# Kernel tuning notes

Hardware: AMD Instinct MI355X
Metric: run time of the kernel (lower is better)

The kernel has to match this reference:

```python
import jax, jax.numpy as jnp
import numpy as np

N_NODES = 100000
N_EDGES = 3200000
IN_DIM = 512
HID_DIM = 16


def spmm(edge_src, edge_dst, edge_weight, feats):
    # out[i] = sum_{(j->i) in E} w_e * feats[j]  (sparse adj @ feats)
    gathered = feats[edge_src] * edge_weight[:, None]  # [E, D]
    return jax.ops.segment_sum(gathered, edge_dst, num_segments=N_NODES)


def setup_inputs() -> dict:
    key = jax.random.key(0)
    ks = jax.random.split(key, 8)
    x = jax.random.normal(ks[0], (N_NODES, IN_DIM), dtype=jnp.float32)
    edge_src = jax.random.randint(ks[1], (N_EDGES,), 0, N_NODES, dtype=jnp.int32)
    edge_dst = jax.random.randint(ks[2], (N_EDGES,), 0, N_NODES, dtype=jnp.int32)
    # normalized adjacency weights (positive, small, like D^-1/2 A D^-1/2 entries)
    edge_weight = jax.random.uniform(ks[3], (N_EDGES,), dtype=jnp.float32) * 0.1
    # Glorot-style init for GraphConvolution weights
    W1 = jax.random.normal(ks[4], (IN_DIM, HID_DIM), dtype=jnp.float32) * (1.0 / np.sqrt(IN_DIM))
    b1 = jnp.zeros((HID_DIM,), dtype=jnp.float32)
    W2 = jax.random.normal(ks[5], (HID_DIM, 1), dtype=jnp.float32) * (1.0 / np.sqrt(HID_DIM))
    b2 = jnp.zeros((1,), dtype=jnp.float32)
    return {"x": x, "edge_src": edge_src, "edge_dst": edge_dst,
            "edge_weight": edge_weight, "W1": W1, "b1": b1, "W2": W2, "b2": b2}


def reference(x, edge_src, edge_dst, edge_weight, W1, b1, W2, b2):
    # Layer 1: GraphConvolution(input_dim -> hidden_dim) + ReLU
    h = spmm(edge_src, edge_dst, edge_weight, x @ W1) + b1  # [N, 16]
    h = jax.nn.relu(h)
    # dropout is identity in eval mode (training=False)
    # Layer 2: GraphConvolution(hidden_dim -> 1)
    out = spmm(edge_src, edge_dst, edge_weight, h @ W2) + b2  # [N, 1]
    return out
```

## Files before the change

### kernel.cpp

```cpp
#include <hip/hip_runtime.h>
#include <hip/hip_fp16.h>

#define N_NODES 100000
#define N_EDGES 3200000
#define IN_DIM  512
#define HID_DIM 16

#define B_BKT   782
#define BKT_SH  7
#define EPB2    5000
#define NBLK2   640
#define CAP_MAX 4608
#define RSTG    9

#define G1_TILES 6250
#define G1_BLK   782
#define MERGED_SMEM 61440

typedef __attribute__((ext_vector_type(8))) short bf16x8;
typedef __attribute__((ext_vector_type(4))) float f32x4;

__device__ __forceinline__ void atomic_add_f32(float* p, float v) {
    __hip_atomic_fetch_add(p, v, __ATOMIC_RELAXED, __HIP_MEMORY_SCOPE_AGENT);
}
__device__ __forceinline__ int atomic_add_i32(int* p, int v) {
    return __hip_atomic_fetch_add(p, v, __ATOMIC_RELAXED, __HIP_MEMORY_SCOPE_AGENT);
}

__device__ __forceinline__ unsigned short bf16_rne(float f) {
    unsigned u = __float_as_uint(f);
    return (unsigned short)((u + 0x7fffu + ((u >> 16) & 1u)) >> 16);
}

__device__ __forceinline__ short bhi(float f) {
    return (short)(__float_as_uint(f) >> 16);
}
__device__ __forceinline__ short blo(float f) {
    float hif = __uint_as_float(__float_as_uint(f) & 0xffff0000u);
    return (short)bf16_rne(f - hif);
}

__device__ __forceinline__ void cvt_hilo(float4 u, float4 v,
                                         bf16x8* __restrict__ hi,
                                         bf16x8* __restrict__ lo) {
    bf16x8 h, l;
    h[0] = bhi(u.x); h[1] = bhi(u.y); h[2] = bhi(u.z); h[3] = bhi(u.w);
    h[4] = bhi(v.x); h[5] = bhi(v.y); h[6] = bhi(v.z); h[7] = bhi(v.w);
    l[0] = blo(u.x); l[1] = blo(u.y); l[2] = blo(u.z); l[3] = blo(u.w);
    l[4] = blo(v.x); l[5] = blo(v.y); l[6] = blo(v.z); l[7] = blo(v.w);
    *hi = h; *lo = l;
}

__device__ __forceinline__ void g1_tile_body(const float* __restrict__ xrow,
                                             const unsigned short* __restrict__ whp,
                                             const unsigned short* __restrict__ wlp,
                                             __half* __restrict__ xwh,
                                             int row0, int lane) {
    f32x4 acc = {0.f, 0.f, 0.f, 0.f};
    float4 a0 = *(const float4*)(xrow);
    float4 a1 = *(const float4*)(xrow + 4);
    float4 b0 = *(const float4*)(xrow + 32);
    float4 b1 = *(const float4*)(xrow + 36);
#pragma unroll
    for (int i = 0; i < 8; ++i) {
        float4 n0, n1, m0, m1;
        if (i < 7) {
            n0 = *(const float4*)(xrow + (2 * i + 2) * 32);
            n1 = *(const float4*)(xrow + (2 * i + 2) * 32 + 4);
            m0 = *(const float4*)(xrow + (2 * i + 3) * 32);
            m1 = *(const float4*)(xrow + (2 * i + 3) * 32 + 4);
        }
        bf16x8 ah, al;
        cvt_hilo(a0, a1, &ah, &al);
        bf16x8 bh = *(const bf16x8*)(whp + (size_t)(2 * i) * 512);
        bf16x8 bl = *(const bf16x8*)(wlp + (size_t)(2 * i) * 512);
        acc = __builtin_amdgcn_mfma_f32_16x16x32_bf16(ah, bh, acc, 0, 0, 0);
        acc = __builtin_amdgcn_mfma_f32_16x16x32_bf16(al, bh, acc, 0, 0, 0);
        acc = __builtin_amdgcn_mfma_f32_16x16x32_bf16(ah, bl, acc, 0, 0, 0);
        cvt_hilo(b0, b1, &ah, &al);
        bh = *(const bf16x8*)(whp + (size_t)(2 * i + 1) * 512);
        bl = *(const bf16x8*)(wlp + (size_t)(2 * i + 1) * 512);
        acc = __builtin_amdgcn_mfma_f32_16x16x32_bf16(ah, bh, acc, 0, 0, 0);
        acc = __builtin_amdgcn_mfma_f32_16x16x32_bf16(al, bh, acc, 0, 0, 0);
        acc = __builtin_amdgcn_mfma_f32_16x16x32_bf16(ah, bl, acc, 0, 0, 0);
        a0 = n0; a1 = n1; b0 = m0; b1 = m1;
    }
    const int n     = lane & 15;
    const int rbase = row0 + ((lane >> 4) << 2);
    xwh[(size_t)(rbase + 0) * HID_DIM + n] = __float2half_rn(acc[0]);
    xwh[(size_t)(rbase + 1) * HID_DIM + n] = __float2half_rn(acc[1]);
    xwh[(size_t)(rbase + 2) * HID_DIM + n] = __float2half_rn(acc[2]);
    xwh[(size_t)(rbase + 3) * HID_DIM + n] = __float2half_rn(acc[3]);
}

__global__ void z0_init(int* __restrict__ cursor, int cap) {
    int b = blockIdx.x * blockDim.x + threadIdx.x;
    if (b < B_BKT) cursor[b] = b * cap;
}

__global__ __launch_bounds__(512) void m1_gs(const float* __restrict__ x,
                                             const float* __restrict__ W1,
                                             __half* __restrict__ xwh,
                                             const int* __restrict__ src,
                                             const int* __restrict__ dst,
                                             const float* __restrict__ wgt,
                                             int* __restrict__ cursor,
                                             uint2* __restrict__ rec, int cap) {
    extern __shared__ __align__(16) char smem[];
    const int t = threadIdx.x;

    if (blockIdx.x < NBLK2) {
        uint2*          srt   = (uint2*)smem;
        unsigned short* bkt   = (unsigned short*)(smem + 40000);
        int*            hist  = (int*)(smem + 50000);
        int*            lbase = (int*)(smem + 53128);
        int*            gbase = (int*)(smem + 56256);
        int*            scn   = (int*)(smem + 59384);

        for (int b = t; b < B_BKT; b += 512) hist[b] = 0;
        __syncthreads();

        const int e0 = blockIdx.x * EPB2;
        const int4*   d4 = (const int4*)(dst + e0);
        const int4*   s4 = (const int4*)(src + e0);
        const float4* w4 = (const float4*)(wgt + e0);
        const int NG = EPB2 / 4;

        for (int g = t; g < NG; g += 512) {
            int4 d = d4[g];
            atomicAdd(&hist[d.x >> BKT_SH], 1);
            atomicAdd(&hist[d.y >> BKT_SH], 1);
            atomicAdd(&hist[d.z >> BKT_SH], 1);
            atomicAdd(&hist[d.w >> BKT_SH], 1);
        }
        __syncthreads();

        int c0 = 0, c1 = 0;
        if (t < 391) { c0 = hist[2 * t]; c1 = hist[2 * t + 1]; }
        int s = c0 + c1;
        scn[t] = s;
        __syncthreads();
        for (int off = 1; off < 512; off <<= 1) {
            int v = (t >= off) ? scn[t - off] : 0;
            __syncthreads();
            scn[t] += v;
            __syncthreads();
        }
        int excl = scn[t] - s;
        if (t < 391) {
            lbase[2 * t]     = excl;
            lbase[2 * t + 1] = excl + c0;
        }
        __syncthreads();

        for (int b = t; b < B_BKT; b += 512) {
            int c = hist[b];
            gbase[b] = c > 0 ? atomic_add_i32(&cursor[b], c) : 0;
        }
        __syncthreads();
        for (int b = t; b < B_BKT; b += 512) hist[b] = lbase[b];
        __syncthreads();

        for (int g = t; g < NG; g += 512) {
            int4 d = d4[g];
            int4 sv = s4[g];
            float4 w = w4[g];
            {
                int b = d.x >> BKT_SH;
                int pos = atomicAdd(&hist[b], 1);
                srt[pos] = make_uint2(((unsigned)sv.x << BKT_SH) | (unsigned)(d.x & 127),
                                      __float_as_uint(w.x));
                bkt[pos] = (unsigned short)b;
            }
            {
                int b = d.y >> BKT_SH;
                int pos = atomicAdd(&hist[b], 1);
                srt[pos] = make_uint2(((unsigned)sv.y << BKT_SH) | (unsigned)(d.y & 127),
                                      __float_as_uint(w.y));
                bkt[pos] = (unsigned short)b;
            }
            {
                int b = d.z >> BKT_SH;
                int pos = atomicAdd(&hist[b], 1);
                srt[pos] = make_uint2(((unsigned)sv.z << BKT_SH) | (unsigned)(d.z & 127),
                                      __float_as_uint(w.z));
                bkt[pos] = (unsigned short)b;
            }
            {
                int b = d.w >> BKT_SH;
                int pos = atomicAdd(&hist[b], 1);
                srt[pos] = make_uint2(((unsigned)sv.w << BKT_SH) | (unsigned)(d.w & 127),
                                      __float_as_uint(w.w));
                bkt[pos] = (unsigned short)b;
            }
        }
        __syncthreads();

        for (int i = t; i < EPB2; i += 512) {
            int b = bkt[i];
            rec[gbase[b] + (i - lbase[b])] = srt[i];
        }
    } else {
        unsigned short* whi = (unsigned short*)smem;
        unsigned short* wlo = (unsigned short*)(smem + 16384);

        for (int idx = t; idx < 16 * 64 * 8; idx += 512) {
            int c  = idx >> 9;
            int l  = (idx >> 3) & 63;
            int tt = idx & 7;
            int k  = c * 32 + ((l >> 4) << 3) + tt;
            int j  = l & 15;
            float w = W1[k * HID_DIM + j];
            unsigned u = __float_as_uint(w);
            float hif = __uint_as_float(u & 0xffff0000u);
            whi[idx] = (unsigned short)(u >> 16);
            wlo[idx] = bf16_rne(w - hif);
        }
        __syncthreads();

        const int lane = t & 63;
        const int wid  = (blockIdx.x - NBLK2) * 8 + (t >> 6);
        if (wid >= G1_TILES) return;
        const int row0 = wid * 16;

        const float* xrow = x + (size_t)(row0 + (lane & 15)) * IN_DIM + ((lane >> 4) << 3);
        g1_tile_body(xrow, &whi[lane * 8], &wlo[lane * 8], xwh, row0, lane);
    }
}

__global__ __launch_bounds__(256) void g1_xw_mfma(const float* __restrict__ x,
                                                  const float* __restrict__ W1,
                                                  __half* __restrict__ xwh) {
    __shared__ alignas(16) unsigned short whi[16 * 64 * 8];
    __shared__ alignas(16) unsigned short wlo[16 * 64 * 8];
    const int t = threadIdx.x;

    for (int idx = t; idx < 16 * 64 * 8; idx += 256) {
        int c  = idx >> 9;
        int l  = (idx >> 3) & 63;
        int tt = idx & 7;
        int k  = c * 32 + ((l >> 4) << 3) + tt;
        int j  = l & 15;
        float w = W1[k * HID_DIM + j];
        unsigned u = __float_as_uint(w);
        float hif = __uint_as_float(u & 0xffff0000u);
        whi[idx] = (unsigned short)(u >> 16);
        wlo[idx] = bf16_rne(w - hif);
    }
    __syncthreads();

    const int lane = t & 63;
    const int wid  = blockIdx.x * 4 + (t >> 6);
    if (wid >= G1_TILES) return;
    const int row0 = wid * 16;

    const float* xrow = x + (size_t)(row0 + (lane & 15)) * IN_DIM + ((lane >> 4) << 3);
    g1_tile_body(xrow, &whi[lane * 8], &wlo[lane * 8], xwh, row0, lane);
}

__global__ __launch_bounds__(512) void s2p4b(const int* __restrict__ cursor,
                                             const uint2* __restrict__ rec,
                                             const __half* __restrict__ xwh,
                                             const float* __restrict__ b1,
                                             const float* __restrict__ W2,
                                             float* __restrict__ hw, int cap) {
    __shared__ uint2 srt[CAP_MAX];
    __shared__ int ocnt[128], scn[128], cur[128];
    const int t = threadIdx.x;
    const int bkt = blockIdx.x;
    const int e0 = bkt * cap;
    int n = cursor[bkt] - e0;
    n = max(0, min(n, cap));
    if (t < 128) ocnt[t] = 0;
    __syncthreads();

    uint2 rg[RSTG];
#pragma unroll
    for (int q = 0; q < RSTG; ++q) {
        int i = t + q * 512;
        if (i < n) {
            rg[q] = rec[e0 + i];
            atomicAdd(&ocnt[rg[q].x & 127u], 1);
        }
    }
    __syncthreads();

    if (t < 128) scn[t] = ocnt[t];
    __syncthreads();
    for (int off = 1; off < 128; off <<= 1) {
        int v = 0;
        if (t < 128 && t >= off) v = scn[t - off];
        __syncthreads();
        if (t < 128 && t >= off) scn[t] += v;
        __syncthreads();
    }
    if (t < 128) cur[t] = scn[t] - ocnt[t];
    __syncthreads();

#pragma unroll
    for (int q = 0; q < RSTG; ++q) {
        int i = t + q * 512;
        if (i < n) {
            uint2 r = rg[q];
            int d = (int)(r.x & 127u);
            int pos = atomicAdd(&cur[d], 1);
            srt[pos] = make_uint2(r.x >> BKT_SH, r.y);
        }
    }
    __syncthreads();

    const int j = t & 15;
    for (int g = (t >> 4); g < 128; g += 32) {
        const int node = (bkt << BKT_SH) + g;
        if (node >= N_NODES) continue;
        int e = scn[g] - ocnt[g];
        const int end = scn[g];
        float acc = 0.0f;
        for (; e + 8 <= end; e += 8) {
            uint2 q0 = srt[e],     q1 = srt[e + 1], q2 = srt[e + 2], q3 = srt[e + 3];
            uint2 q4 = srt[e + 4], q5 = srt[e + 5], q6 = srt[e + 6], q7 = srt[e + 7];
            float f0 = __half2float(xwh[(size_t)q0.x * HID_DIM + j]);
            float f1 = __half2float(xwh[(size_t)q1.x * HID_DIM + j]);
            float f2 = __half2float(xwh[(size_t)q2.x * HID_DIM + j]);
            float f3 = __half2float(xwh[(size_t)q3.x * HID_DIM + j]);
            float f4 = __half2float(xwh[(size_t)q4.x * HID_DIM + j]);
            float f5 = __half2float(xwh[(size_t)q5.x * HID_DIM + j]);
            float f6 = __half2float(xwh[(size_t)q6.x * HID_DIM + j]);
            float f7 = __half2float(xwh[(size_t)q7.x * HID_DIM + j]);
            acc += __uint_as_float(q0.y) * f0;
            acc += __uint_as_float(q1.y) * f1;
            acc += __uint_as_float(q2.y) * f2;
            acc += __uint_as_float(q3.y) * f3;
            acc += __uint_as_float(q4.y) * f4;
            acc += __uint_as_float(q5.y) * f5;
            acc += __uint_as_float(q6.y) * f6;
            acc += __uint_as_float(q7.y) * f7;
        }
        for (; e + 4 <= end; e += 4) {
            uint2 q0 = srt[e], q1 = srt[e + 1], q2 = srt[e + 2], q3 = srt[e + 3];
            float f0 = __half2float(xwh[(size_t)q0.x * HID_DIM + j]);
            float f1 = __half2float(xwh[(size_t)q1.x * HID_DIM + j]);
            float f2 = __half2float(xwh[(size_t)q2.x * HID_DIM + j]);
            float f3 = __half2float(xwh[(size_t)q3.x * HID_DIM + j]);
            acc += __uint_as_float(q0.y) * f0;
            acc += __uint_as_float(q1.y) * f1;
            acc += __uint_as_float(q2.y) * f2;
            acc += __uint_as_float(q3.y) * f3;
        }
        for (; e < end; ++e) {
            uint2 q = srt[e];
            acc += __uint_as_float(q.y) * __half2float(xwh[(size_t)q.x * HID_DIM + j]);
        }
        float v = fmaxf(acc + b1[j], 0.0f) * W2[j];
        v += __shfl_xor(v, 1);
        v += __shfl_xor(v, 2);
        v += __shfl_xor(v, 4);
        v += __shfl_xor(v, 8);
        if (j == 0) hw[node] = v;
    }
}

__global__ __launch_bounds__(512) void p5c(const int* __restrict__ cursor,
                                           const uint2* __restrict__ rec,
                                           const float* __restrict__ hwv,
                                           const float* __restrict__ b2,
                                           float* __restrict__ out, int cap) {
    __shared__ float o[128];
    const int t = threadIdx.x;
    const int bkt = blockIdx.x;
    const int e0 = bkt * cap;
    int n = cursor[bkt] - e0;
    n = max(0, min(n, cap));
    if (t < 128) o[t] = 0.0f;
    __syncthreads();
    const uint4* r4 = (const uint4*)(rec + e0);
    const int m = n >> 1;
    for (int i = t; i < m; i += 512) {
        uint4 q = r4[i];
        float v0 = __uint_as_float(q.y) * hwv[q.x >> BKT_SH];
        float v1 = __uint_as_float(q.w) * hwv[q.z >> BKT_SH];
        atomicAdd(&o[q.x & 127u], v0);
        atomicAdd(&o[q.z & 127u], v1);
    }
    if ((n & 1) && t == 0) {
        uint2 q = rec[e0 + n - 1];
        atomicAdd(&o[q.x & 127u], __uint_as_float(q.y) * hwv[q.x >> BKT_SH]);
    }
    __syncthreads();
    if (t < 128) {
        int node = (bkt << BKT_SH) + t;
        if (node < N_NODES) out[node] = b2[0] + o[t];
    }
}

__global__ void f0_zero(float* __restrict__ h, const float* __restrict__ b2,
                        float* __restrict__ out) {
    int i = blockIdx.x * blockDim.x + threadIdx.x;
    if (i < N_NODES * HID_DIM) h[i] = 0.0f;
    if (i < N_NODES) out[i] = b2[0];
}
__global__ void k2_spmm1(const int* __restrict__ src, const int* __restrict__ dst,
                         const float* __restrict__ wgt, const __half* __restrict__ xwh,
                         float* __restrict__ h) {
    int t = blockIdx.x * blockDim.x + threadIdx.x;
    int e = t >> 4;
    int j = t & (HID_DIM - 1);
    if (e < N_EDGES) {
        float v = wgt[e] * __half2float(xwh[(size_t)src[e] * HID_DIM + j]);
        atomic_add_f32(&h[(size_t)dst[e] * HID_DIM + j], v);
    }
}
__global__ void k3_act(const float* __restrict__ h, const float* __restrict__ b1,
                       const float* __restrict__ W2, float* __restrict__ hw) {
    int i = blockIdx.x * blockDim.x + threadIdx.x;
    if (i >= N_NODES) return;
    const float4* h4 = (const float4*)(h + (size_t)i * HID_DIM);
    const float4* b4 = (const float4*)b1;
    const float4* w4 = (const float4*)W2;
    float acc = 0.0f;
#pragma unroll
    for (int q = 0; q < HID_DIM / 4; ++q) {
        float4 hv = h4[q]; float4 bv = b4[q]; float4 wv = w4[q];
        acc += fmaxf(hv.x + bv.x, 0.0f) * wv.x;
        acc += fmaxf(hv.y + bv.y, 0.0f) * wv.y;
        acc += fmaxf(hv.z + bv.z, 0.0f) * wv.z;
        acc += fmaxf(hv.w + bv.w, 0.0f) * wv.w;
    }
    hw[i] = acc;
}
__global__ void k4_spmm2(const int* __restrict__ src, const int* __restrict__ dst,
                         const float* __restrict__ wgt, const float* __restrict__ hw,
                         float* __restrict__ out) {
    int e = blockIdx.x * blockDim.x + threadIdx.x;
    if (e < N_EDGES) atomic_add_f32(&out[dst[e]], wgt[e] * hw[src[e]]);
}


extern "C" void kernel_launch(void* const* d_in, const int* in_sizes, int n_in,
                              void* d_out, int out_size, void* d_ws, size_t ws_size,
                              hipStream_t stream) {
    const float* x    = (const float*)d_in[0];
    const int*   esrc = (const int*)  d_in[1];
    const int*   edst = (const int*)  d_in[2];
    const float* ew   = (const float*)d_in[3];
    const float* W1   = (const float*)d_in[4];
    const float* b1   = (const float*)d_in[5];
    const float* W2   = (const float*)d_in[6];
    const float* b2   = (const float*)d_in[7];
    float* out = (float*)d_out;
    char* ws = (char*)d_ws;

    __half* xwh    = (__half*)ws;
    float*  hw     = (float*)(ws + (size_t)N_NODES * HID_DIM * 2);
    int*    cursor = (int*)(hw + N_NODES);
    int2*   row    = (int2*)(((size_t)(cursor + B_BKT) + 7) & ~(size_t)7);
    size_t rec_off = ((size_t)((char*)(row + N_NODES) - ws) + 15) & ~(size_t)15;
    uint2* rec = (uint2*)(ws + rec_off);
    (void)row;

    int cap = 0;
    if (ws_size > rec_off) {
        size_t cap_fit = (ws_size - rec_off) / ((size_t)B_BKT * sizeof(uint2));
        cap = (int)(cap_fit < CAP_MAX ? cap_fit : CAP_MAX);
    }

    if (cap >= 4480) {
        z0_init<<<(B_BKT + 255) / 256, 256, 0, stream>>>(cursor, cap);
        m1_gs<<<NBLK2 + G1_BLK, 512, MERGED_SMEM, stream>>>(x, W1, xwh,
                                                            esrc, edst, ew,
                                                            cursor, rec, cap);
        s2p4b<<<B_BKT, 512, 0, stream>>>(cursor, rec, xwh, b1, W2, hw, cap);
        p5c<<<B_BKT, 512, 0, stream>>>(cursor, rec, hw, b2, out, cap);
    } else {
        __half* f_xwh = (__half*)ws;
        float*  f_h   = (float*)(ws + (size_t)N_NODES * HID_DIM * 2);
        float*  f_hw  = f_h + (size_t)N_NODES * HID_DIM;
        int n = N_NODES * HID_DIM;
        f0_zero<<<(n + 255) / 256, 256, 0, stream>>>(f_h, b2, out);
        g1_xw_mfma<<<(G1_TILES + 3) / 4, 256, 0, stream>>>(x, W1, f_xwh);
        k2_spmm1<<<(N_EDGES * 16) / 256, 256, 0, stream>>>(esrc, edst, ew, f_xwh, f_h);
        k3_act<<<(N_NODES + 255) / 256, 256, 0, stream>>>(f_h, b1, W2, f_hw);
        k4_spmm2<<<(N_EDGES + 255) / 256, 256, 0, stream>>>(esrc, edst, ew, f_hw, out);
    }
}
```

Before: 395.9 us.

## Split GEMM tile K-dimension across four waves with LDS reduction in merged kernel

In the merged sort/GEMM kernel, each 16-row tile of x@W1 is now computed by four waves, each covering a 128-wide K slice, instead of one wave covering all of K. Partial accumulators are written to shared memory and summed by the first wave, which writes the fp16 output. The GEMM block count grows from 782 to 3125, with 2 tiles per block instead of 8. The aim is more loads in flight and shorter per-wave dependency chains for the memory-bound x read, at the cost of a block barrier, LDS traffic, and repeating the W1 hi/lo split in four times as many blocks.

```diff
diff --git a/kernel.cpp b/kernel.cpp
--- a/kernel.cpp
+++ b/kernel.cpp
@@ -14,7 +14,7 @@
 #define RSTG    9
 
 #define G1_TILES 6250
-#define G1_BLK   782
+#define G1_BLK2  3125
 #define MERGED_SMEM 61440
 
 typedef __attribute__((ext_vector_type(8))) short bf16x8;
@@ -31,7 +31,6 @@
     unsigned u = __float_as_uint(f);
     return (unsigned short)((u + 0x7fffu + ((u >> 16) & 1u)) >> 16);
 }
-
 __device__ __forceinline__ short bhi(float f) {
     return (short)(__float_as_uint(f) >> 16);
 }
@@ -39,7 +38,6 @@
     float hif = __uint_as_float(__float_as_uint(f) & 0xffff0000u);
     return (short)bf16_rne(f - hif);
 }
-
 __device__ __forceinline__ void cvt_hilo(float4 u, float4 v,
                                          bf16x8* __restrict__ hi,
                                          bf16x8* __restrict__ lo) {
@@ -49,48 +47,6 @@
     l[0] = blo(u.x); l[1] = blo(u.y); l[2] = blo(u.z); l[3] = blo(u.w);
     l[4] = blo(v.x); l[5] = blo(v.y); l[6] = blo(v.z); l[7] = blo(v.w);
     *hi = h; *lo = l;
-}
-
-__device__ __forceinline__ void g1_tile_body(const float* __restrict__ xrow,
-                                             const unsigned short* __restrict__ whp,
-                                             const unsigned short* __restrict__ wlp,
-                                             __half* __restrict__ xwh,
-                                             int row0, int lane) {
-    f32x4 acc = {0.f, 0.f, 0.f, 0.f};
-    float4 a0 = *(const float4*)(xrow);
-    float4 a1 = *(const float4*)(xrow + 4);
-    float4 b0 = *(const float4*)(xrow + 32);
-    float4 b1 = *(const float4*)(xrow + 36);
-#pragma unroll
-    for (int i = 0; i < 8; ++i) {
-        float4 n0, n1, m0, m1;
-        if (i < 7) {
-            n0 = *(const float4*)(xrow + (2 * i + 2) * 32);
-            n1 = *(const float4*)(xrow + (2 * i + 2) * 32 + 4);
-            m0 = *(const float4*)(xrow + (2 * i + 3) * 32);
-            m1 = *(const float4*)(xrow + (2 * i + 3) * 32 + 4);
-        }
-        bf16x8 ah, al;
-        cvt_hilo(a0, a1, &ah, &al);
-        bf16x8 bh = *(const bf16x8*)(whp + (size_t)(2 * i) * 512);
-        bf16x8 bl = *(const bf16x8*)(wlp + (size_t)(2 * i) * 512);
-        acc = __builtin_amdgcn_mfma_f32_16x16x32_bf16(ah, bh, acc, 0, 0, 0);
-        acc = __builtin_amdgcn_mfma_f32_16x16x32_bf16(al, bh, acc, 0, 0, 0);
-        acc = __builtin_amdgcn_mfma_f32_16x16x32_bf16(ah, bl, acc, 0, 0, 0);
-        cvt_hilo(b0, b1, &ah, &al);
-        bh = *(const bf16x8*)(whp + (size_t)(2 * i + 1) * 512);
-        bl = *(const bf16x8*)(wlp + (size_t)(2 * i + 1) * 512);
-        acc = __builtin_amdgcn_mfma_f32_16x16x32_bf16(ah, bh, acc, 0, 0, 0);
-        acc = __builtin_amdgcn_mfma_f32_16x16x32_bf16(al, bh, acc, 0, 0, 0);
-        acc = __builtin_amdgcn_mfma_f32_16x16x32_bf16(ah, bl, acc, 0, 0, 0);
-        a0 = n0; a1 = n1; b0 = m0; b1 = m1;
-    }
-    const int n     = lane & 15;
-    const int rbase = row0 + ((lane >> 4) << 2);
-    xwh[(size_t)(rbase + 0) * HID_DIM + n] = __float2half_rn(acc[0]);
-    xwh[(size_t)(rbase + 1) * HID_DIM + n] = __float2half_rn(acc[1]);
-    xwh[(size_t)(rbase + 2) * HID_DIM + n] = __float2half_rn(acc[2]);
-    xwh[(size_t)(rbase + 3) * HID_DIM + n] = __float2half_rn(acc[3]);
 }
 
 __global__ void z0_init(int* __restrict__ cursor, int cap) {
@@ -201,8 +157,9 @@
             rec[gbase[b] + (i - lbase[b])] = srt[i];
         }
     } else {
-        unsigned short* whi = (unsigned short*)smem;
-        unsigned short* wlo = (unsigned short*)(smem + 16384);
+        unsigned short* whi  = (unsigned short*)smem;
+        unsigned short* wlo  = (unsigned short*)(smem + 16384);
+        f32x4*          part = (f32x4*)(smem + 32768);
 
         for (int idx = t; idx < 16 * 64 * 8; idx += 512) {
             int c  = idx >> 9;
@@ -219,12 +176,69 @@
         __syncthreads();
 
         const int lane = t & 63;
-        const int wid  = (blockIdx.x - NBLK2) * 8 + (t >> 6);
-        if (wid >= G1_TILES) return;
+        const int wave = t >> 6;
+        const int tl   = wave >> 2;
+        const int ks   = wave & 3;
+        const int wid  = (blockIdx.x - NBLK2) * 2 + tl;
         const int row0 = wid * 16;
 
-        const float* xrow = x + (size_t)(row0 + (lane & 15)) * IN_DIM + ((lane >> 4) << 3);
-        g1_tile_body(xrow, &whi[lane * 8], &wlo[lane * 8], xwh, row0, lane);
+        const float* xrow = x + (size_t)(row0 + (lane & 15)) * IN_DIM
+                              + ((lane >> 4) << 3) + ks * 128;
+
+        float4 c0a = *(const float4*)(xrow);
+        float4 c0b = *(const float4*)(xrow + 4);
+        float4 c1a = *(const float4*)(xrow + 32);
+        float4 c1b = *(const float4*)(xrow + 36);
+        float4 c2a = *(const float4*)(xrow + 64);
+        float4 c2b = *(const float4*)(xrow + 68);
+        float4 c3a = *(const float4*)(xrow + 96);
+        float4 c3b = *(const float4*)(xrow + 100);
+
+        const unsigned short* whp = &whi[(size_t)(ks * 4) * 512 + lane * 8];
+        const unsigned short* wlp = &wlo[(size_t)(ks * 4) * 512 + lane * 8];
+
+        f32x4 acc = {0.f, 0.f, 0.f, 0.f};
+        bf16x8 ah, al, bh, bl;
+        cvt_hilo(c0a, c0b, &ah, &al);
+        bh = *(const bf16x8*)(whp);
+        bl = *(const bf16x8*)(wlp);
+        acc = __builtin_amdgcn_mfma_f32_16x16x32_bf16(ah, bh, acc, 0, 0, 0);
+        acc = __builtin_amdgcn_mfma_f32_16x16x32_bf16(al, bh, acc, 0, 0, 0);
+        acc = __builtin_amdgcn_mfma_f32_16x16x32_bf16(ah, bl, acc, 0, 0, 0);
+        cvt_hilo(c1a, c1b, &ah, &al);
+        bh = *(const bf16x8*)(whp + 512);
+        bl = *(const bf16x8*)(wlp + 512);
+        acc = __builtin_amdgcn_mfma_f32_16x16x32_bf16(ah, bh, acc, 0, 0, 0);
+        acc = __builtin_amdgcn_mfma_f32_16x16x32_bf16(al, bh, acc, 0, 0, 0);
+        acc = __builtin_amdgcn_mfma_f32_16x16x32_bf16(ah, bl, acc, 0, 0, 0);
+        cvt_hilo(c2a, c2b, &ah, &al);
+        bh = *(const bf16x8*)(whp + 1024);
+        bl = *(const bf16x8*)(wlp + 1024);
+        acc = __builtin_amdgcn_mfma_f32_16x16x32_bf16(ah, bh, acc, 0, 0, 0);
+        acc = __builtin_amdgcn_mfma_f32_16x16x32_bf16(al, bh, acc, 0, 0, 0);
+        acc = __builtin_amdgcn_mfma_f32_16x16x32_bf16(ah, bl, acc, 0, 0, 0);
+        cvt_hilo(c3a, c3b, &ah, &al);
+        bh = *(const bf16x8*)(whp + 1536);
+        bl = *(const bf16x8*)(wlp + 1536);
+        acc = __builtin_amdgcn_mfma_f32_16x16x32_bf16(ah, bh, acc, 0, 0, 0);
+        acc = __builtin_amdgcn_mfma_f32_16x16x32_bf16(al, bh, acc, 0, 0, 0);
+        acc = __builtin_amdgcn_mfma_f32_16x16x32_bf16(ah, bl, acc, 0, 0, 0);
+
+        part[(size_t)wave * 64 + lane] = acc;
+        __syncthreads();
+        if (ks == 0) {
+            f32x4 p0 = part[(size_t)(tl * 4 + 0) * 64 + lane];
+            f32x4 p1 = part[(size_t)(tl * 4 + 1) * 64 + lane];
+            f32x4 p2 = part[(size_t)(tl * 4 + 2) * 64 + lane];
+            f32x4 p3 = part[(size_t)(tl * 4 + 3) * 64 + lane];
+            f32x4 sum = ((p0 + p1) + p2) + p3;
+            const int n     = lane & 15;
+            const int rbase = row0 + ((lane >> 4) << 2);
+            xwh[(size_t)(rbase + 0) * HID_DIM + n] = __float2half_rn(sum[0]);
+            xwh[(size_t)(rbase + 1) * HID_DIM + n] = __float2half_rn(sum[1]);
+            xwh[(size_t)(rbase + 2) * HID_DIM + n] = __float2half_rn(sum[2]);
+            xwh[(size_t)(rbase + 3) * HID_DIM + n] = __float2half_rn(sum[3]);
+        }
     }
 }
 
@@ -255,7 +269,44 @@
     const int row0 = wid * 16;
 
     const float* xrow = x + (size_t)(row0 + (lane & 15)) * IN_DIM + ((lane >> 4) << 3);
-    g1_tile_body(xrow, &whi[lane * 8], &wlo[lane * 8], xwh, row0, lane);
+    const unsigned short* whp = &whi[lane * 8];
+    const unsigned short* wlp = &wlo[lane * 8];
+
+    f32x4 acc = {0.f, 0.f, 0.f, 0.f};
+    float4 a0 = *(const float4*)(xrow);
+    float4 a1 = *(const float4*)(xrow + 4);
+    float4 b0 = *(const float4*)(xrow + 32);
+    float4 b1 = *(const float4*)(xrow + 36);
+#pragma unroll
+    for (int i = 0; i < 8; ++i) {
+        float4 n0, n1, m0, m1;
+        if (i < 7) {
+            n0 = *(const float4*)(xrow + (2 * i + 2) * 32);
+            n1 = *(const float4*)(xrow + (2 * i + 2) * 32 + 4);
+            m0 = *(const float4*)(xrow + (2 * i + 3) * 32);
+            m1 = *(const float4*)(xrow + (2 * i + 3) * 32 + 4);
+        }
+        bf16x8 ah, al;
+        cvt_hilo(a0, a1, &ah, &al);
+        bf16x8 bh = *(const bf16x8*)(whp + (size_t)(2 * i) * 512);
+        bf16x8 bl = *(const bf16x8*)(wlp + (size_t)(2 * i) * 512);
+        acc = __builtin_amdgcn_mfma_f32_16x16x32_bf16(ah, bh, acc, 0, 0, 0);
+        acc = __builtin_amdgcn_mfma_f32_16x16x32_bf16(al, bh, acc, 0, 0, 0);
+        acc = __builtin_amdgcn_mfma_f32_16x16x32_bf16(ah, bl, acc, 0, 0, 0);
+        cvt_hilo(b0, b1, &ah, &al);
+        bh = *(const bf16x8*)(whp + (size_t)(2 * i + 1) * 512);
+        bl = *(const bf16x8*)(wlp + (size_t)(2 * i + 1) * 512);
+        acc = __builtin_amdgcn_mfma_f32_16x16x32_bf16(ah, bh, acc, 0, 0, 0);
+        acc = __builtin_amdgcn_mfma_f32_16x16x32_bf16(al, bh, acc, 0, 0, 0);
+        acc = __builtin_amdgcn_mfma_f32_16x16x32_bf16(ah, bl, acc, 0, 0, 0);
+        a0 = n0; a1 = n1; b0 = m0; b1 = m1;
+    }
+    const int n     = lane & 15;
+    const int rbase = row0 + ((lane >> 4) << 2);
+    xwh[(size_t)(rbase + 0) * HID_DIM + n] = __float2half_rn(acc[0]);
+    xwh[(size_t)(rbase + 1) * HID_DIM + n] = __float2half_rn(acc[1]);
+    xwh[(size_t)(rbase + 2) * HID_DIM + n] = __float2half_rn(acc[2]);
+    xwh[(size_t)(rbase + 3) * HID_DIM + n] = __float2half_rn(acc[3]);
 }
 
 __global__ __launch_bounds__(512) void s2p4b(const int* __restrict__ cursor,
@@ -466,9 +517,9 @@
 
     if (cap >= 4480) {
         z0_init<<<(B_BKT + 255) / 256, 256, 0, stream>>>(cursor, cap);
-        m1_gs<<<NBLK2 + G1_BLK, 512, MERGED_SMEM, stream>>>(x, W1, xwh,
-                                                            esrc, edst, ew,
-                                                            cursor, rec, cap);
+        m1_gs<<<NBLK2 + G1_BLK2, 512, MERGED_SMEM, stream>>>(x, W1, xwh,
+                                                             esrc, edst, ew,
+                                                             cursor, rec, cap);
         s2p4b<<<B_BKT, 512, 0, stream>>>(cursor, rec, xwh, b1, W2, hw, cap);
         p5c<<<B_BKT, 512, 0, stream>>>(cursor, rec, hw, b2, out, cap);
     } else {
```

Result: no change. 390.5 us (-1.4%).
